# Performance work log

Measured on AMD Instinct MI355X. Metric: run time of the kernel, lower is better.

The kernel has to match this reference:

```python
import jax, jax.numpy as jnp
import numpy as np

B, T, D, H, DH, W = 2, 2048, 512, 8, 64, 64  # batch, seq, d_model, heads, d_head, window
BASE = 10000.0


def rope(x):
    # x: [b, t, d]; rotate-half RoPE applied over the full feature dim (as in source: pos_enc on d_model)
    d = x.shape[-1]
    half = d // 2
    inv_freq = BASE ** (-jnp.arange(half, dtype=jnp.float32) / half)          # [half]
    ang = jnp.arange(x.shape[1], dtype=jnp.float32)[:, None] * inv_freq       # [t, half]
    cos, sin = jnp.cos(ang), jnp.sin(ang)
    x1, x2 = x[..., :half], x[..., half:]
    return jnp.concatenate([x1 * cos - x2 * sin, x1 * sin + x2 * cos], axis=-1)


def setup_inputs() -> dict:
    key = jax.random.key(0)
    k0, k1, k2, k3 = jax.random.split(key, 4)
    x = jax.random.normal(k0, (B, T, D), jnp.float32)
    Wq = jax.random.normal(k1, (D, D), jnp.float32) / jnp.sqrt(D)
    Wkv = jax.random.normal(k2, (D, 2 * D), jnp.float32) / jnp.sqrt(D)
    # NOTE: source zero-inits lin; we use random weights so the output/grads are non-trivial
    Wlin = jax.random.normal(k3, (D, D), jnp.float32) / jnp.sqrt(D)
    blin = jnp.zeros((D,), jnp.float32)
    return {"x": x, "Wq": Wq, "Wkv": Wkv, "Wlin": Wlin, "blin": blin}


def reference(x, Wq, Wkv, Wlin, blin):
    b, t, _ = x.shape
    scale = DH ** -0.5
    q = rope(x @ Wq).reshape(b, t, H, DH).transpose(0, 2, 1, 3)               # [b,h,t,d]
    kv = x @ Wkv
    k, v = kv[..., :D], kv[..., D:]
    k = rope(k).reshape(b, t, H, DH).transpose(0, 2, 1, 3)                    # [b,h,t,d]
    v = v.reshape(b, t, H, DH).transpose(0, 2, 1, 3)                          # [b,h,t,d]
    pad = [(0, 0), (0, 0), (W - 1, 0), (0, 0)]
    kp, vp = jnp.pad(k, pad), jnp.pad(v, pad)                                 # [b,h,t+W-1,d]
    idx = jnp.arange(t)[:, None] + jnp.arange(W)[None, :]                     # [t,W] sliding-window gather
    kw, vw = kp[:, :, idx], vp[:, :, idx]                                     # [b,h,t,W,d]
    attn = jax.nn.softmax(jnp.einsum('bhtd,bhtwd->bhtw', q, kw) * scale, axis=-1)
    out = jnp.einsum('bhtw,bhtwd->bhtd', attn, vw)                            # [b,h,t,d]
    out = out.transpose(0, 2, 1, 3).reshape(b, t, D)
    return out @ Wlin + blin
```

## Files before the change

### kernel.cpp

```cpp
#include <hip/hip_runtime.h>
#include <cstddef>

#define T_N 2048
#define M_N 4096
#define KW  512

typedef __attribute__((ext_vector_type(4))) float f32x4;
typedef _Float16 f16x8 __attribute__((ext_vector_type(8)));
typedef _Float16 f16x2 __attribute__((ext_vector_type(2)));

#define GLOAD_LDS(g, l) __builtin_amdgcn_global_load_lds( \
    (const __attribute__((address_space(1))) unsigned int*)(g), \
    (__attribute__((address_space(3))) unsigned int*)(l), 16, 0, 0)

__global__ __launch_bounds__(256) void prep(
    const float* __restrict__ x, const float* __restrict__ Wq,
    const float* __restrict__ Wkv, const float* __restrict__ Wlin,
    _Float16* __restrict__ Axp, _Float16* __restrict__ Wcatp,
    _Float16* __restrict__ Wlinp, _Float16* __restrict__ tab16) {
  __shared__ float tile[64][65];
  const int bid = blockIdx.x;
  const int tid = threadIdx.x;
  if (bid < 1024) {
    int idx = bid * 256 + tid;
    int m = idx >> 6, k8 = (idx & 63) << 3;
    const float* src = x + (size_t)m * 512 + k8;
    const float4 a = *(const float4*)src;
    const float4 b = *(const float4*)(src + 4);
    f16x8 o;
    o[0] = (_Float16)a.x; o[1] = (_Float16)a.y; o[2] = (_Float16)a.z; o[3] = (_Float16)a.w;
    o[4] = (_Float16)b.x; o[5] = (_Float16)b.y; o[6] = (_Float16)b.z; o[7] = (_Float16)b.w;
    *(f16x8*)(Axp + (size_t)m * 512 + k8) = o;
    return;
  }
  if (bid >= 1280) {
    int gid = (bid - 1280) * 256 + tid;
    int t = gid >> 8, f = gid & 255;
    float invf = exp2f(-0.05190512648261503f * (float)f);
    float s, c;
    sincosf((float)t * invf, &s, &c);
    f16x2 cs;
    cs[0] = (_Float16)c; cs[1] = (_Float16)s;
    *(f16x2*)(tab16 + 2 * ((size_t)t * 256 + f)) = cs;
    return;
  }
  int wb = bid - 1024;
  const float* W; int N; int mode; int bx, by;
  if (wb < 64)       { W = Wq;   N = 512;  mode = 0; bx = wb & 7;  by = wb >> 3; }
  else if (wb < 192) { wb -= 64;  W = Wkv; N = 1024; mode = 1; bx = wb & 15; by = wb >> 4; }
  else               { wb -= 192; W = Wlin; N = 512; mode = 2; bx = wb & 7;  by = wb >> 3; }
  const int n0 = bx * 64, k0 = by * 64;
#pragma unroll
  for (int it = 0; it < 16; ++it) {
    int idx = tid + it * 256;
    int r = idx >> 6, c = idx & 63;
    tile[r][c] = W[(size_t)(k0 + r) * N + n0 + c];
  }
  __syncthreads();
#pragma unroll
  for (int it = 0; it < 16; ++it) {
    int idx = tid + it * 256;
    int n = idx >> 6, kk = idx & 63;
    int cg = n0 + n;
    int np; _Float16* out;
    if (mode == 0)      { np = 2 * (cg & 255) + (cg >> 8); out = Wcatp; }
    else if (mode == 1) { np = (cg < 512) ? 512 + 2 * (cg & 255) + (cg >> 8)
                                          : 1024 + (cg - 512);
                          out = Wcatp; }
    else                { np = cg; out = Wlinp; }
    out[(size_t)np * KW + k0 + kk] = (_Float16)tile[kk][n];
  }
}

__global__ __launch_bounds__(256) void gemm_qkv_rope(
    const _Float16* __restrict__ Ap, const _Float16* __restrict__ Bp,
    const _Float16* __restrict__ tab16, _Float16* __restrict__ Qh,
    _Float16* __restrict__ Kh, _Float16* __restrict__ Vn) {
  __shared__ __align__(16) _Float16 sA[64 * 64];
  __shared__ __align__(16) _Float16 sB[128 * 64];
  const int tid = threadIdx.x;
  const int wid = tid >> 6, lane = tid & 63;
  const int il = lane & 15, g = lane >> 4;
  const int m0 = blockIdx.y * 64, n0 = blockIdx.x * 128;
  const int wm = (wid >> 1) * 32, wn = (wid & 1) * 64;
  f32x4 acc[2][4] = {};

  const _Float16* ga = Ap + (size_t)(m0 + wid * 16 + (lane >> 3)) * KW + (lane & 7) * 8;
  const _Float16* gb = Bp + (size_t)(n0 + wid * 32 + (lane >> 3)) * KW + (lane & 7) * 8;
  _Float16* la = sA + wid * 16 * 64;
  _Float16* lb = sB + wid * 32 * 64;

  for (int k0 = 0; k0 < KW; k0 += 64) {
    GLOAD_LDS(ga + k0, la);
    GLOAD_LDS(ga + 8 * KW + k0, la + 8 * 64);
#pragma unroll
    for (int p = 0; p < 4; ++p)
      GLOAD_LDS(gb + (size_t)(p * 8) * KW + k0, lb + p * 8 * 64);
    __syncthreads();
#pragma unroll
    for (int ks = 0; ks < 2; ++ks) {
      f16x8 af[2], bf[4];
#pragma unroll
      for (int i = 0; i < 2; ++i)
        af[i] = *(const f16x8*)&sA[(wm + i * 16 + il) * 64 + ks * 32 + g * 8];
#pragma unroll
      for (int j = 0; j < 4; ++j)
        bf[j] = *(const f16x8*)&sB[(wn + j * 16 + il) * 64 + ks * 32 + g * 8];
#pragma unroll
      for (int i = 0; i < 2; ++i)
#pragma unroll
        for (int j = 0; j < 4; ++j)
          acc[i][j] = __builtin_amdgcn_mfma_f32_16x16x32_f16(af[i], bf[j], acc[i][j], 0, 0, 0);
    }
    __syncthreads();
  }
  const int b8 = (m0 >> 11) * 8;
  const bool isv = (n0 >= 1024);
  const bool isk = (n0 >= 512) && !isv;
  const int n0p = n0 - (isk ? 512 : 0);
#pragma unroll
  for (int i = 0; i < 2; ++i) {
#pragma unroll
    for (int j = 0; j < 4; ++j) {
      f32x4 v = acc[i][j];
#pragma unroll
      for (int r = 0; r < 4; ++r) {
        float self = v[r];
        float part = __shfl_xor(self, 1);
        int tl = wm + i * 16 + g * 4 + r;
        int tpos = (m0 + tl) & (T_N - 1);
        if (isv) {
          Vn[(size_t)(m0 + tl) * 512 + (n0 - 1024) + wn + il + 16 * j] = (_Float16)self;
        } else {
          int p = il & 1;
          int f = (n0p + wn + 16 * j + (il & 14)) >> 1;
          f16x2 cs = *(const f16x2*)(tab16 + 2 * ((size_t)tpos * 256 + f));
          float c = (float)cs[0], s = (float)cs[1];
          float o = p ? (self * c + part * s) : (self * c - part * s);
          int h = (f >> 6) + (p << 2);
          int d = f & 63;
          _Float16* dst = isk ? Kh : Qh;
          dst[((size_t)(b8 + h) * T_N + tpos) * 64 + d] = (_Float16)o;
        }
      }
    }
  }
}

__global__ __launch_bounds__(256) void vtrans(
    const _Float16* __restrict__ Vn, _Float16* __restrict__ Vh) {
  __shared__ _Float16 vt[64][72];
  const int bid = blockIdx.x;
  const int tid = threadIdx.x;
  const int b = bid >> 8, h = (bid >> 5) & 7, tt = bid & 31;
  const int t0 = tt * 64;
#pragma unroll
  for (int it = 0; it < 16; ++it) {
    int idx = tid + it * 256;
    int tl = idx >> 6, d = idx & 63;
    vt[d][tl] = Vn[(size_t)(b * T_N + t0 + tl) * 512 + h * 64 + d];
  }
  __syncthreads();
#pragma unroll
  for (int it = 0; it < 2; ++it) {
    int idx = tid + it * 256;
    int d = idx >> 3, tc = (idx & 7) * 8;
    *(f16x8*)(Vh + ((size_t)(b * 8 + h) * 64 + d) * T_N + t0 + tc) =
        *(const f16x8*)&vt[d][tc];
  }
}

#define RQ 72
#define RK 72
#define RV 104
#define RP 104
#define RO 72

__global__ __launch_bounds__(256, 4) void attn_fused(
    const _Float16* __restrict__ Qh, const _Float16* __restrict__ Kh,
    const _Float16* __restrict__ Vh, _Float16* __restrict__ Aout) {
  __shared__ __align__(16) _Float16 sm[19200];
  __shared__ float pm[2][32];
  __shared__ float ps[2][32];
  _Float16* Ks  = sm;
  _Float16* Qs  = sm + 6912;
  _Float16* VTs = sm + 9216;
  _Float16* Ps  = sm + 15872;
  _Float16* OH  = sm;

  const int wgid = blockIdx.x;
  const int orig = (wgid & 7) * 128 + (wgid >> 3);
  const int tile = orig & 63;
  const int h = (orig >> 6) & 7;
  const int b = orig >> 9;
  const int t0 = tile * 32;
  const int tid = threadIdx.x;
  const size_t bh = (size_t)(b * 8 + h);

  {
    int i = tid >> 3, d8 = (tid & 7) * 8;
    *(f16x8*)(Qs + i * RQ + d8) =
        *(const f16x8*)(Qh + (bh * T_N + t0 + i) * 64 + d8);
  }
#pragma unroll
  for (int itn = 0; itn < 3; ++itn) {
    int c = tid + itn * 256;
    int jr = c >> 3, d8 = (c & 7) * 8;
    int p = t0 - 64 + jr;
    f16x8 o = {};
    if (p >= 0) o = *(const f16x8*)(Kh + (bh * T_N + p) * 64 + d8);
    *(f16x8*)(Ks + jr * RK + d8) = o;
  }
#pragma unroll
  for (int itn = 0; itn < 3; ++itn) {
    int c = tid + itn * 256;
    int d = c & 63, jr8 = (c >> 6) * 8;
    int p8 = t0 - 64 + jr8;
    f16x8 o = {};
    if (p8 >= 0) o = *(const f16x8*)(Vh + (bh * 64 + d) * T_N + p8);
    *(f16x8*)(VTs + d * RV + jr8) = o;
  }
  __syncthreads();

  const int lane = tid & 63;
  const int il = lane & 15, g = lane >> 4;
  const int w = tid >> 6;
  const int it = w & 1, jh = w >> 1;
  const int i_q = 16 * it + il;

  f32x4 sacc[3] = {};
  {
    f16x8 qf0 = *(const f16x8*)(Qs + i_q * RQ + 8 * g);
    f16x8 qf1 = *(const f16x8*)(Qs + i_q * RQ + 32 + 8 * g);
#pragma unroll
    for (int jt = 0; jt < 3; ++jt) {
      int jrow = 16 * (3 * jh + jt) + il;
      f16x8 a0 = *(const f16x8*)(Ks + jrow * RK + 8 * g);
      f16x8 a1 = *(const f16x8*)(Ks + jrow * RK + 32 + 8 * g);
      sacc[jt] = __builtin_amdgcn_mfma_f32_16x16x32_f16(a0, qf0, sacc[jt], 0, 0, 0);
      sacc[jt] = __builtin_amdgcn_mfma_f32_16x16x32_f16(a1, qf1, sacc[jt], 0, 0, 0);
    }
  }
  float mx = -3e38f;
#pragma unroll
  for (int jt = 0; jt < 3; ++jt)
#pragma unroll
    for (int r = 0; r < 4; ++r) {
      int j = 16 * (3 * jh + jt) + 4 * g + r;
      int wv = j - 1 - i_q;
      if (wv >= 0 && wv < 64) mx = fmaxf(mx, sacc[jt][r]);
    }
  mx = fmaxf(mx, __shfl_xor(mx, 16));
  mx = fmaxf(mx, __shfl_xor(mx, 32));
  if (g == 0) pm[jh][i_q] = mx;
  __syncthreads();
  {
    const float m = fmaxf(pm[0][i_q], pm[1][i_q]);
    float sum = 0.f;
#pragma unroll
    for (int jt = 0; jt < 3; ++jt)
#pragma unroll
      for (int r = 0; r < 4; ++r) {
        int j = 16 * (3 * jh + jt) + 4 * g + r;
        int wv = j - 1 - i_q;
        float ex = 0.f;
        if (wv >= 0 && wv < 64) {
          ex = exp2f((sacc[jt][r] - m) * 0.18033688011112042f);
          sum += ex;
        }
        Ps[i_q * RP + j] = (_Float16)ex;
      }
    sum += __shfl_xor(sum, 16);
    sum += __shfl_xor(sum, 32);
    if (g == 0) ps[jh][i_q] = sum;
  }
  __syncthreads();

  f32x4 oacc[2] = {};
#pragma unroll
  for (int ks = 0; ks < 3; ++ks) {
    f16x8 pf = *(const f16x8*)(Ps + i_q * RP + 32 * ks + 8 * g);
#pragma unroll
    for (int q2 = 0; q2 < 2; ++q2) {
      int dt = jh + 2 * q2;
      f16x8 vf = *(const f16x8*)(VTs + (16 * dt + il) * RV + 32 * ks + 8 * g);
      oacc[q2] = __builtin_amdgcn_mfma_f32_16x16x32_f16(pf, vf, oacc[q2], 0, 0, 0);
    }
  }
#pragma unroll
  for (int r = 0; r < 4; ++r) {
    int i = 16 * it + 4 * g + r;
    float inv = 1.f / (ps[0][i] + ps[1][i]);
#pragma unroll
    for (int q2 = 0; q2 < 2; ++q2) {
      int d = 16 * (jh + 2 * q2) + il;
      OH[i * RO + d] = (_Float16)(oacc[q2][r] * inv);
    }
  }
  __syncthreads();
  {
    int i = tid >> 3, d8 = (tid & 7) * 8;
    *(f16x8*)(Aout + ((size_t)(b * T_N + t0 + i)) * 512 + h * 64 + d8) =
        *(const f16x8*)(OH + i * RO + d8);
  }
}

__global__ __launch_bounds__(256) void gemm_out(
    const _Float16* __restrict__ Ap, const _Float16* __restrict__ Bp,
    const float* __restrict__ bias, float* __restrict__ C) {
  __shared__ __align__(16) _Float16 sA[64 * 64];
  __shared__ __align__(16) _Float16 sB[64 * 64];
  const int tid = threadIdx.x;
  const int wid = tid >> 6, lane = tid & 63;
  const int il = lane & 15, g = lane >> 4;
  const int m0 = blockIdx.y * 64, n0 = blockIdx.x * 64;
  const int wm = (wid >> 1) * 32, wn = (wid & 1) * 32;
  f32x4 acc[2][2] = {};

  const _Float16* ga = Ap + (size_t)(m0 + wid * 16 + (lane >> 3)) * KW + (lane & 7) * 8;
  const _Float16* gb = Bp + (size_t)(n0 + wid * 16 + (lane >> 3)) * KW + (lane & 7) * 8;
  _Float16* la = sA + wid * 16 * 64;
  _Float16* lb = sB + wid * 16 * 64;

  for (int k0 = 0; k0 < KW; k0 += 64) {
    GLOAD_LDS(ga + k0, la);
    GLOAD_LDS(ga + 8 * KW + k0, la + 8 * 64);
    GLOAD_LDS(gb + k0, lb);
    GLOAD_LDS(gb + 8 * KW + k0, lb + 8 * 64);
    __syncthreads();
#pragma unroll
    for (int ks = 0; ks < 2; ++ks) {
      f16x8 af[2], bf[2];
#pragma unroll
      for (int i = 0; i < 2; ++i)
        af[i] = *(const f16x8*)&sA[(wm + i * 16 + il) * 64 + ks * 32 + g * 8];
#pragma unroll
      for (int j = 0; j < 2; ++j)
        bf[j] = *(const f16x8*)&sB[(wn + j * 16 + il) * 64 + ks * 32 + g * 8];
#pragma unroll
      for (int i = 0; i < 2; ++i)
#pragma unroll
        for (int j = 0; j < 2; ++j)
          acc[i][j] = __builtin_amdgcn_mfma_f32_16x16x32_f16(af[i], bf[j], acc[i][j], 0, 0, 0);
    }
    __syncthreads();
  }
  const int cn = n0 + wn + il;
  const int rbase = m0 + wm + g * 4;
#pragma unroll
  for (int j = 0; j < 2; ++j) {
    float badd = bias[cn + j * 16];
#pragma unroll
    for (int i = 0; i < 2; ++i)
#pragma unroll
      for (int r = 0; r < 4; ++r)
        C[(size_t)(rbase + i * 16 + r) * 512 + cn + j * 16] = acc[i][j][r] + badd;
  }
}

extern "C" void kernel_launch(void* const* d_in, const int* in_sizes, int n_in,
                              void* d_out, int out_size, void* d_ws, size_t ws_size,
                              hipStream_t stream) {
  const float* x    = (const float*)d_in[0];
  const float* Wq   = (const float*)d_in[1];
  const float* Wkv  = (const float*)d_in[2];
  const float* Wlin = (const float*)d_in[3];
  const float* blin = (const float*)d_in[4];
  float* out = (float*)d_out;

  char* ws = (char*)d_ws;
  _Float16* Axp   = (_Float16*)(ws);
  _Float16* Wcatp = (_Float16*)(ws + 4194304);
  _Float16* Wlinp = (_Float16*)(ws + 5767168);
  _Float16* tab16 = (_Float16*)(ws + 6291456);
  _Float16* Qh    = (_Float16*)(ws + 8388608);
  _Float16* Kh    = (_Float16*)(ws + 12582912);
  _Float16* Vn    = (_Float16*)(ws + 16777216);
  _Float16* Vh    = (_Float16*)(ws + 20971520);
  _Float16* Aaop  = (_Float16*)(ws + 25165824);

  prep<<<3328, 256, 0, stream>>>(x, Wq, Wkv, Wlin, Axp, Wcatp, Wlinp, tab16);
  gemm_qkv_rope<<<dim3(12, 64), 256, 0, stream>>>(Axp, Wcatp, tab16, Qh, Kh, Vn);
  vtrans<<<512, 256, 0, stream>>>(Vn, Vh);
  attn_fused<<<1024, 256, 0, stream>>>(Qh, Kh, Vh, Aaop);
  gemm_out<<<dim3(8, 64), 256, 0, stream>>>(Aaop, Wlinp, blin, out);
}
```

Measured before the change: 112.0 us.

## Fuse V transpose into QKV GEMM epilogue and stage Q/K stores through LDS

The separate vtrans kernel is removed. The QKV GEMM epilogue now writes V already transposed into head-major layout, staging it through shared memory and issuing 16-byte stores. The Q/K RoPE outputs are also staged in LDS and written as coalesced 16-byte rows instead of scattered 2-byte stores. This cuts one launch and a round trip of V through global memory, at the cost of extra LDS traffic and a barrier in the epilogue.

```diff
diff --git a/kernel.cpp b/kernel.cpp
--- a/kernel.cpp
+++ b/kernel.cpp
@@ -75,9 +75,10 @@
 __global__ __launch_bounds__(256) void gemm_qkv_rope(
     const _Float16* __restrict__ Ap, const _Float16* __restrict__ Bp,
     const _Float16* __restrict__ tab16, _Float16* __restrict__ Qh,
-    _Float16* __restrict__ Kh, _Float16* __restrict__ Vn) {
-  __shared__ __align__(16) _Float16 sA[64 * 64];
-  __shared__ __align__(16) _Float16 sB[128 * 64];
+    _Float16* __restrict__ Kh, _Float16* __restrict__ Vh) {
+  __shared__ __align__(16) _Float16 sm[64 * 64 + 128 * 64];
+  _Float16* sA = sm;
+  _Float16* sB = sm + 64 * 64;
   const int tid = threadIdx.x;
   const int wid = tid >> 6, lane = tid & 63;
   const int il = lane & 15, g = lane >> 4;
@@ -115,9 +116,39 @@
     __syncthreads();
   }
   const int b8 = (m0 >> 11) * 8;
+  const int tb = m0 & (T_N - 1);
   const bool isv = (n0 >= 1024);
   const bool isk = (n0 >= 512) && !isv;
+  _Float16* OT  = sm;
+  _Float16* OTV = sm;
+
+  if (isv) {
+#pragma unroll
+    for (int i = 0; i < 2; ++i)
+#pragma unroll
+      for (int j = 0; j < 4; ++j) {
+        f32x4 v = acc[i][j];
+        int col = wn + 16 * j + il;
+#pragma unroll
+        for (int r = 0; r < 4; ++r) {
+          int tl = wm + i * 16 + g * 4 + r;
+          OTV[col * 72 + tl] = (_Float16)v[r];
+        }
+      }
+    __syncthreads();
+    const int cv = n0 - 1024;
+#pragma unroll
+    for (int it = 0; it < 4; ++it) {
+      int c = tid + it * 256;
+      int col = c >> 3, t8 = (c & 7) * 8;
+      int h = (cv + col) >> 6, d = (cv + col) & 63;
+      *(f16x8*)(Vh + ((size_t)(b8 + h) * 64 + d) * T_N + tb + t8) =
+          *(const f16x8*)&OTV[col * 72 + t8];
+    }
+    return;
+  }
   const int n0p = n0 - (isk ? 512 : 0);
+  const int h0 = n0p >> 7;
 #pragma unroll
   for (int i = 0; i < 2; ++i) {
 #pragma unroll
@@ -128,45 +159,24 @@
         float self = v[r];
         float part = __shfl_xor(self, 1);
         int tl = wm + i * 16 + g * 4 + r;
-        int tpos = (m0 + tl) & (T_N - 1);
-        if (isv) {
-          Vn[(size_t)(m0 + tl) * 512 + (n0 - 1024) + wn + il + 16 * j] = (_Float16)self;
-        } else {
-          int p = il & 1;
-          int f = (n0p + wn + 16 * j + (il & 14)) >> 1;
-          f16x2 cs = *(const f16x2*)(tab16 + 2 * ((size_t)tpos * 256 + f));
-          float c = (float)cs[0], s = (float)cs[1];
-          float o = p ? (self * c + part * s) : (self * c - part * s);
-          int h = (f >> 6) + (p << 2);
-          int d = f & 63;
-          _Float16* dst = isk ? Kh : Qh;
-          dst[((size_t)(b8 + h) * T_N + tpos) * 64 + d] = (_Float16)o;
-        }
+        int tpos = tb + tl;
+        int p = il & 1;
+        int f = (n0p + wn + 16 * j + (il & 14)) >> 1;
+        f16x2 cs = *(const f16x2*)(tab16 + 2 * ((size_t)tpos * 256 + f));
+        float c = (float)cs[0], s = (float)cs[1];
+        float o = p ? (self * c + part * s) : (self * c - part * s);
+        OT[(p * 64 + tl) * 72 + (f & 63)] = (_Float16)o;
       }
     }
   }
-}
-
-__global__ __launch_bounds__(256) void vtrans(
-    const _Float16* __restrict__ Vn, _Float16* __restrict__ Vh) {
-  __shared__ _Float16 vt[64][72];
-  const int bid = blockIdx.x;
-  const int tid = threadIdx.x;
-  const int b = bid >> 8, h = (bid >> 5) & 7, tt = bid & 31;
-  const int t0 = tt * 64;
-#pragma unroll
-  for (int it = 0; it < 16; ++it) {
-    int idx = tid + it * 256;
-    int tl = idx >> 6, d = idx & 63;
-    vt[d][tl] = Vn[(size_t)(b * T_N + t0 + tl) * 512 + h * 64 + d];
-  }
-  __syncthreads();
-#pragma unroll
-  for (int it = 0; it < 2; ++it) {
-    int idx = tid + it * 256;
-    int d = idx >> 3, tc = (idx & 7) * 8;
-    *(f16x8*)(Vh + ((size_t)(b * 8 + h) * 64 + d) * T_N + t0 + tc) =
-        *(const f16x8*)&vt[d][tc];
+  __syncthreads();
+  _Float16* dst = isk ? Kh : Qh;
+#pragma unroll
+  for (int it = 0; it < 4; ++it) {
+    int c = tid + it * 256;
+    int p = c >> 9, row = (c >> 3) & 63, d8 = (c & 7) * 8;
+    *(f16x8*)(dst + ((size_t)(b8 + h0 + 4 * p) * T_N + tb + row) * 64 + d8) =
+        *(const f16x8*)&OT[(p * 64 + row) * 72 + d8];
   }
 }
 
@@ -375,13 +385,11 @@
   _Float16* tab16 = (_Float16*)(ws + 6291456);
   _Float16* Qh    = (_Float16*)(ws + 8388608);
   _Float16* Kh    = (_Float16*)(ws + 12582912);
-  _Float16* Vn    = (_Float16*)(ws + 16777216);
-  _Float16* Vh    = (_Float16*)(ws + 20971520);
-  _Float16* Aaop  = (_Float16*)(ws + 25165824);
+  _Float16* Vh    = (_Float16*)(ws + 16777216);
+  _Float16* Aaop  = (_Float16*)(ws + 20971520);
 
   prep<<<3328, 256, 0, stream>>>(x, Wq, Wkv, Wlin, Axp, Wcatp, Wlinp, tab16);
-  gemm_qkv_rope<<<dim3(12, 64), 256, 0, stream>>>(Axp, Wcatp, tab16, Qh, Kh, Vn);
-  vtrans<<<512, 256, 0, stream>>>(Vn, Vh);
+  gemm_qkv_rope<<<dim3(12, 64), 256, 0, stream>>>(Axp, Wcatp, tab16, Qh, Kh, Vh);
   attn_fused<<<1024, 256, 0, stream>>>(Qh, Kh, Vh, Aaop);
   gemm_out<<<dim3(8, 64), 256, 0, stream>>>(Aaop, Wlinp, blin, out);
 }
```

Result: faster. 104.1 us (-7.1%).
